# Performance work log

Measured on AMD Instinct MI355X. Metric: run time of the kernel, lower is better.

## Reference

```python
import jax, jax.numpy as jnp
import numpy as np

TOP_K = 2  # num_experts_per_tok


def setup_inputs() -> dict:
    key = jax.random.key(0)
    k1, k2, k3, k4 = jax.random.split(key, 4)
    T, H, I, E = 1024, 2048, 768, 8  # tokens, hidden, moe_intermediate, num_experts
    return {
        "hidden_states": jax.random.normal(k1, (T, H), jnp.float32),
        "gate_w": jax.random.normal(k2, (E, H), jnp.float32) * 0.02,      # router nn.Linear(H,E) weight
        "w_gate_up": jax.random.normal(k3, (E, 2 * I, H), jnp.float32) * 0.02,  # merged gate+up proj per expert
        "w_down": jax.random.normal(k4, (E, H, I), jnp.float32) * 0.02,   # down proj per expert
    }


def _moe(hidden_states, gate_w, w_gate_up, w_down):
    T, H = hidden_states.shape
    E = gate_w.shape[0]
    # router: softmax in fp32, then top-k, renormalize (matches _forward_local)
    logits = hidden_states @ gate_w.T                         # [T, E]
    probs = jax.nn.softmax(logits.astype(jnp.float32), axis=-1)
    top_w, top_i = jax.lax.top_k(probs, TOP_K)                # [T, K]
    top_w = top_w / jnp.sum(top_w, axis=-1, keepdims=True)
    top_w = top_w.astype(hidden_states.dtype)
    # per-token combine weight for each expert (top-k indices are unique per token)
    comb = jnp.zeros((T, E), hidden_states.dtype).at[
        jnp.arange(T)[:, None], top_i
    ].add(top_w)                                              # [T, E]

    def body(acc, xs):
        wgu, wd, cw = xs            # [2I,H], [H,I], [T]
        gu = hidden_states @ wgu.T  # [T, 2I]
        g, u = jnp.split(gu, 2, axis=-1)
        h = jax.nn.silu(g) * u      # SiluAndMul
        out = h @ wd.T              # [T, H]
        return acc + out * cw[:, None], None

    init = jnp.zeros_like(hidden_states)
    out, _ = jax.lax.scan(body, init, (w_gate_up, w_down, comb.T))
    return out


def reference(hidden_states, gate_w, w_gate_up, w_down):
    return _moe(hidden_states, gate_w, w_gate_up, w_down)
```

## Files before the change

kernel.cpp:

```cpp
#include <hip/hip_runtime.h>
#include <hip/hip_bf16.h>

typedef unsigned short u16;
typedef __bf16 bf16x8 __attribute__((ext_vector_type(8)));
typedef float f32x4 __attribute__((ext_vector_type(4)));

#define T_TOK 1024
#define HID   2048
#define IMM   768
#define NE    8
#define TWOI  1536
#define KTOT  6144

static __device__ __forceinline__ u16 f2bf(float f) {
  unsigned u = __float_as_uint(f);
  u += 0x7FFFu + ((u >> 16) & 1u);
  return (u16)(u >> 16);
}
static __device__ __forceinline__ float bf2f(u16 s) {
  return __uint_as_float(((unsigned)s) << 16);
}

__global__ __launch_bounds__(64) void router_kernel(
    const float* __restrict__ hid, const float* __restrict__ gw,
    float* __restrict__ comb)
{
  const int t = blockIdx.x;
  const int lane = threadIdx.x;
  float acc[NE];
#pragma unroll
  for (int e = 0; e < NE; ++e) acc[e] = 0.f;
  const float4* h4 = (const float4*)(hid + (long)t * HID);
#pragma unroll 2
  for (int c = lane; c < HID / 4; c += 64) {
    float4 x = h4[c];
#pragma unroll
    for (int e = 0; e < NE; ++e) {
      float4 w = ((const float4*)(gw + e * HID))[c];
      acc[e] += x.x * w.x + x.y * w.y + x.z * w.z + x.w * w.w;
    }
  }
#pragma unroll
  for (int e = 0; e < NE; ++e) {
    float v = acc[e];
#pragma unroll
    for (int off = 32; off > 0; off >>= 1) v += __shfl_xor(v, off, 64);
    acc[e] = v;
  }
  if (lane == 0) {
    float mx = acc[0];
#pragma unroll
    for (int e = 1; e < NE; ++e) mx = fmaxf(mx, acc[e]);
    float p[NE]; float s = 0.f;
#pragma unroll
    for (int e = 0; e < NE; ++e) { p[e] = expf(acc[e] - mx); s += p[e]; }
    const float inv = 1.f / s;
    float p1 = -1.f, p2 = -1.f; int i1 = 0, i2 = 0;
#pragma unroll
    for (int e = 0; e < NE; ++e) {
      float pe = p[e] * inv;
      if (pe > p1)      { p2 = p1; i2 = i1; p1 = pe; i1 = e; }
      else if (pe > p2) { p2 = pe; i2 = e; }
    }
    const float wsum = p1 + p2;
    float cw[NE];
#pragma unroll
    for (int e = 0; e < NE; ++e) cw[e] = 0.f;
    cw[i1] = p1 / wsum;
    cw[i2] = p2 / wsum;
#pragma unroll
    for (int e = 0; e < NE; ++e) comb[t * NE + e] = cw[e];
  }
}

__global__ __launch_bounds__(256) void cvt_kernel(
    const float* __restrict__ in, u16* __restrict__ out)
{
  const int i = blockIdx.x * 256 + threadIdx.x;
  float4 x = ((const float4*)in)[i];
  ushort4 o;
  o.x = f2bf(x.x); o.y = f2bf(x.y); o.z = f2bf(x.z); o.w = f2bf(x.w);
  ((ushort4*)out)[i] = o;
}

template<int K, bool OUT_ATOMIC>
__global__ __launch_bounds__(256, 2) void gemm_bt(
    const u16* __restrict__ A, int lda, long a_zoff,
    const float* __restrict__ B, long b_zoff,
    u16* __restrict__ Cb, float* __restrict__ Cf, int ldc, long c_zoff)
{
  constexpr int BM = 128, BN = 128, BK = 32;
  constexpr int LSTR = BK + 8;
  constexpr int NKT = K / BK;
  static_assert(NKT >= 2 && (K % BK) == 0, "K must be multiple of 32, >=64");
  __shared__ __align__(16) u16 As[2][BM * LSTR];
  __shared__ __align__(16) u16 Bs[2][BN * LSTR];

  const int tid  = threadIdx.x;
  const int lane = tid & 63;
  const int wave = tid >> 6;
  const int wm = wave >> 1, wn = wave & 1;
  const int lrow = lane & 15;
  const int lk   = (lane >> 4) << 3;

  const int z = blockIdx.z;
  const long m0 = (long)blockIdx.x * BM;
  const long n0 = (long)blockIdx.y * BN;

  const u16*   Ab = A + a_zoff * z + m0 * lda;
  const float* Bb = B + b_zoff * z + n0 * (long)K;

  const int r0  = tid >> 2;
  const int cs0 = (tid & 3) << 3;

  uint4 sa0, sa1; float4 sb0a, sb0b, sb1a, sb1b;

  auto gload = [&](int kk) {
    const u16* ap = Ab + (long)r0 * lda + kk + cs0;
    sa0 = *(const uint4*)ap;
    sa1 = *(const uint4*)(ap + 64l * lda);
    const float* bp = Bb + (long)r0 * K + kk + cs0;
    sb0a = *(const float4*)bp;
    sb0b = *(const float4*)(bp + 4);
    sb1a = *(const float4*)(bp + 64l * K);
    sb1b = *(const float4*)(bp + 64l * K + 4);
  };
  auto packb = [&](const float4& f0, const float4& f1) -> uint4 {
    return make_uint4(
      (unsigned)f2bf(f0.x) | ((unsigned)f2bf(f0.y) << 16),
      (unsigned)f2bf(f0.z) | ((unsigned)f2bf(f0.w) << 16),
      (unsigned)f2bf(f1.x) | ((unsigned)f2bf(f1.y) << 16),
      (unsigned)f2bf(f1.z) | ((unsigned)f2bf(f1.w) << 16));
  };
  auto swrite = [&](int buf) {
    *(uint4*)&As[buf][r0 * LSTR + cs0]        = sa0;
    *(uint4*)&As[buf][(r0 + 64) * LSTR + cs0] = sa1;
    *(uint4*)&Bs[buf][r0 * LSTR + cs0]        = packb(sb0a, sb0b);
    *(uint4*)&Bs[buf][(r0 + 64) * LSTR + cs0] = packb(sb1a, sb1b);
  };

  f32x4 acc[4][4];
  const f32x4 zero4 = {0.f, 0.f, 0.f, 0.f};
#pragma unroll
  for (int m = 0; m < 4; ++m)
#pragma unroll
    for (int n = 0; n < 4; ++n) acc[m][n] = zero4;

  auto compute = [&](int buf) {
    bf16x8 af[4], bfr[4];
#pragma unroll
    for (int m = 0; m < 4; ++m)
      af[m] = *(const bf16x8*)&As[buf][(wm * 64 + m * 16 + lrow) * LSTR + lk];
#pragma unroll
    for (int n = 0; n < 4; ++n)
      bfr[n] = *(const bf16x8*)&Bs[buf][(wn * 64 + n * 16 + lrow) * LSTR + lk];
#pragma unroll
    for (int m = 0; m < 4; ++m)
#pragma unroll
      for (int n = 0; n < 4; ++n)
        acc[m][n] = __builtin_amdgcn_mfma_f32_16x16x32_bf16(af[m], bfr[n], acc[m][n], 0, 0, 0);
  };

  gload(0);
  swrite(0);
  __syncthreads();
  int cur = 0;
#pragma unroll 1
  for (int kt = 0; kt < NKT - 1; ++kt) {
    gload((kt + 1) * BK);
    compute(cur);
    swrite(cur ^ 1);
    __syncthreads();
    cur ^= 1;
  }
  compute(cur);

  const long rbase = m0 + wm * 64 + ((lane >> 4) << 2);
  const long cbase = n0 + wn * 64 + lrow;
#pragma unroll
  for (int m = 0; m < 4; ++m) {
#pragma unroll
    for (int n = 0; n < 4; ++n) {
#pragma unroll
      for (int j = 0; j < 4; ++j) {
        const long row = rbase + m * 16 + j;
        const long col = cbase + n * 16;
        if constexpr (OUT_ATOMIC) {
          atomicAdd(Cf + c_zoff * z + row * ldc + col, acc[m][n][j]);
        } else {
          Cb[c_zoff * z + row * ldc + col] = f2bf(acc[m][n][j]);
        }
      }
    }
  }
}

__global__ __launch_bounds__(256) void silu_kernel(
    const u16* __restrict__ gu, const float* __restrict__ comb,
    u16* __restrict__ hp)
{
  const int c = blockIdx.x * 256 + threadIdx.x;
  const int o0 = c << 3;
  const int t = o0 / KTOT;
  const int r = o0 - t * KTOT;
  const int e = r / IMM;
  const int i0 = r - e * IMM;
  const u16* gp = gu + ((long)(e * T_TOK + t) * TWOI) + i0;
  uint4 gv = *(const uint4*)gp;
  uint4 uv = *(const uint4*)(gp + IMM);
  const float cw = comb[t * NE + e];
  const unsigned* gwv = (const unsigned*)&gv;
  const unsigned* uwv = (const unsigned*)&uv;
  unsigned outw[4];
#pragma unroll
  for (int q = 0; q < 4; ++q) {
    float g0 = bf2f((u16)(gwv[q] & 0xFFFFu));
    float g1 = bf2f((u16)(gwv[q] >> 16));
    float u0 = bf2f((u16)(uwv[q] & 0xFFFFu));
    float u1 = bf2f((u16)(uwv[q] >> 16));
    float h0 = cw * u0 * (g0 / (1.f + __expf(-g0)));
    float h1 = cw * u1 * (g1 / (1.f + __expf(-g1)));
    outw[q] = (unsigned)f2bf(h0) | ((unsigned)f2bf(h1) << 16);
  }
  *(uint4*)(hp + (long)o0) = make_uint4(outw[0], outw[1], outw[2], outw[3]);
}

extern "C" void kernel_launch(void* const* d_in, const int* in_sizes, int n_in,
                              void* d_out, int out_size, void* d_ws, size_t ws_size,
                              hipStream_t stream) {
  const float* hid = (const float*)d_in[0];
  const float* gw  = (const float*)d_in[1];
  const float* wgu = (const float*)d_in[2];
  const float* wd  = (const float*)d_in[3];
  float* out = (float*)d_out;

  char* ws = (char*)d_ws;
  u16*   hidb = (u16*)ws;
  float* comb = (float*)(ws + (4l << 20));
  u16*   gu   = (u16*)(ws + (4l << 20) + (1l << 15));
  u16*   hp   = (u16*)(ws + (4l << 20) + (1l << 15)
                          + (long)NE * T_TOK * TWOI * 2);

  hipMemsetAsync(d_out, 0, (size_t)out_size * sizeof(float), stream);
  router_kernel<<<T_TOK, 64, 0, stream>>>(hid, gw, comb);
  cvt_kernel<<<(T_TOK * HID / 4) / 256, 256, 0, stream>>>(hid, hidb);
  gemm_bt<HID, false><<<dim3(T_TOK / 128, TWOI / 128, NE), 256, 0, stream>>>(
      hidb, HID, 0, wgu, (long)TWOI * HID, gu, nullptr, TWOI, (long)T_TOK * TWOI);
  silu_kernel<<<(T_TOK * KTOT / 8) / 256, 256, 0, stream>>>(gu, comb, hp);
  gemm_bt<IMM, true><<<dim3(T_TOK / 128, HID / 128, NE), 256, 0, stream>>>(
      hp, KTOT, IMM, wd, (long)HID * IMM, nullptr, out, HID, 0);
}
```

Measured before the change: 382.1 us.

## Route tokens sparsely to experts with gathered grouped GEMMs instead of dense compute

The router now uses atomic counters to build per-expert token lists and per-slot combine weights, replacing the dense T×E combine matrix. The gate/up GEMM gathers only routed token rows, and grid tiles beyond each expert's count exit early. The SiLU stage works per slot, and the down GEMM scatters atomically into each token's output row. This removes the compute on tokens whose combine weight is zero, about three quarters of the GEMM work with top-2 of 8, at the cost of an extra memset, index indirection and possible load imbalance across experts.

```diff
diff --git a/kernel.cpp b/kernel.cpp
--- a/kernel.cpp
+++ b/kernel.cpp
@@ -10,7 +10,6 @@
 #define IMM   768
 #define NE    8
 #define TWOI  1536
-#define KTOT  6144
 
 static __device__ __forceinline__ u16 f2bf(float f) {
   unsigned u = __float_as_uint(f);
@@ -23,7 +22,7 @@
 
 __global__ __launch_bounds__(64) void router_kernel(
     const float* __restrict__ hid, const float* __restrict__ gw,
-    float* __restrict__ comb)
+    int* __restrict__ cnt, int* __restrict__ tok_of, float* __restrict__ wslot)
 {
   const int t = blockIdx.x;
   const int lane = threadIdx.x;
@@ -63,13 +62,12 @@
       else if (pe > p2) { p2 = pe; i2 = e; }
     }
     const float wsum = p1 + p2;
-    float cw[NE];
-#pragma unroll
-    for (int e = 0; e < NE; ++e) cw[e] = 0.f;
-    cw[i1] = p1 / wsum;
-    cw[i2] = p2 / wsum;
-#pragma unroll
-    for (int e = 0; e < NE; ++e) comb[t * NE + e] = cw[e];
+    int s1 = atomicAdd(&cnt[i1], 1);
+    tok_of[i1 * T_TOK + s1] = t;
+    wslot[i1 * T_TOK + s1] = p1 / wsum;
+    int s2 = atomicAdd(&cnt[i2], 1);
+    tok_of[i2 * T_TOK + s2] = t;
+    wslot[i2 * T_TOK + s2] = p2 / wsum;
   }
 }
 
@@ -83,16 +81,23 @@
   ((ushort4*)out)[i] = o;
 }
 
-template<int K, bool OUT_ATOMIC>
-__global__ __launch_bounds__(256, 2) void gemm_bt(
+template<int K, bool GATHER_A, bool OUT_ATOMIC>
+__global__ __launch_bounds__(256, 2) void gemm_moe(
     const u16* __restrict__ A, int lda, long a_zoff,
     const float* __restrict__ B, long b_zoff,
+    const int* __restrict__ tok_of, const int* __restrict__ cnt,
     u16* __restrict__ Cb, float* __restrict__ Cf, int ldc, long c_zoff)
 {
   constexpr int BM = 128, BN = 128, BK = 32;
   constexpr int LSTR = BK + 8;
   constexpr int NKT = K / BK;
   static_assert(NKT >= 2 && (K % BK) == 0, "K must be multiple of 32, >=64");
+
+  const int z = blockIdx.z;
+  const int nrow = cnt[z];
+  const long m0 = (long)blockIdx.x * BM;
+  if (m0 >= nrow) return;
+
   __shared__ __align__(16) u16 As[2][BM * LSTR];
   __shared__ __align__(16) u16 Bs[2][BN * LSTR];
 
@@ -103,22 +108,26 @@
   const int lrow = lane & 15;
   const int lk   = (lane >> 4) << 3;
 
-  const int z = blockIdx.z;
-  const long m0 = (long)blockIdx.x * BM;
   const long n0 = (long)blockIdx.y * BN;
-
-  const u16*   Ab = A + a_zoff * z + m0 * lda;
   const float* Bb = B + b_zoff * z + n0 * (long)K;
 
   const int r0  = tid >> 2;
   const int cs0 = (tid & 3) << 3;
 
+  const u16 *ap0, *ap1;
+  if constexpr (GATHER_A) {
+    ap0 = A + (long)tok_of[z * T_TOK + m0 + r0] * lda + cs0;
+    ap1 = A + (long)tok_of[z * T_TOK + m0 + r0 + 64] * lda + cs0;
+  } else {
+    ap0 = A + a_zoff * z + (m0 + r0) * (long)lda + cs0;
+    ap1 = ap0 + 64l * lda;
+  }
+
   uint4 sa0, sa1; float4 sb0a, sb0b, sb1a, sb1b;
 
   auto gload = [&](int kk) {
-    const u16* ap = Ab + (long)r0 * lda + kk + cs0;
-    sa0 = *(const uint4*)ap;
-    sa1 = *(const uint4*)(ap + 64l * lda);
+    sa0 = *(const uint4*)(ap0 + kk);
+    sa1 = *(const uint4*)(ap1 + kk);
     const float* bp = Bb + (long)r0 * K + kk + cs0;
     sb0a = *(const float4*)bp;
     sb0b = *(const float4*)(bp + 4);
@@ -175,7 +184,7 @@
   }
   compute(cur);
 
-  const long rbase = m0 + wm * 64 + ((lane >> 4) << 2);
+  const int rloc = wm * 64 + ((lane >> 4) << 2);
   const long cbase = n0 + wn * 64 + lrow;
 #pragma unroll
   for (int m = 0; m < 4; ++m) {
@@ -183,12 +192,15 @@
     for (int n = 0; n < 4; ++n) {
 #pragma unroll
       for (int j = 0; j < 4; ++j) {
-        const long row = rbase + m * 16 + j;
+        const long slot = m0 + rloc + m * 16 + j;
         const long col = cbase + n * 16;
         if constexpr (OUT_ATOMIC) {
-          atomicAdd(Cf + c_zoff * z + row * ldc + col, acc[m][n][j]);
+          if (slot < nrow) {
+            const long tok = tok_of[z * T_TOK + slot];
+            atomicAdd(Cf + tok * ldc + col, acc[m][n][j]);
+          }
         } else {
-          Cb[c_zoff * z + row * ldc + col] = f2bf(acc[m][n][j]);
+          Cb[c_zoff * z + slot * ldc + col] = f2bf(acc[m][n][j]);
         }
       }
     }
@@ -196,19 +208,17 @@
 }
 
 __global__ __launch_bounds__(256) void silu_kernel(
-    const u16* __restrict__ gu, const float* __restrict__ comb,
+    const u16* __restrict__ gu, const float* __restrict__ wslot,
     u16* __restrict__ hp)
 {
   const int c = blockIdx.x * 256 + threadIdx.x;
-  const int o0 = c << 3;
-  const int t = o0 / KTOT;
-  const int r = o0 - t * KTOT;
-  const int e = r / IMM;
-  const int i0 = r - e * IMM;
-  const u16* gp = gu + ((long)(e * T_TOK + t) * TWOI) + i0;
+  const int idx = c << 3;
+  const int g = idx / IMM;
+  const int i0 = idx - g * IMM;
+  const u16* gp = gu + (long)g * TWOI + i0;
   uint4 gv = *(const uint4*)gp;
   uint4 uv = *(const uint4*)(gp + IMM);
-  const float cw = comb[t * NE + e];
+  const float cw = wslot[g];
   const unsigned* gwv = (const unsigned*)&gv;
   const unsigned* uwv = (const unsigned*)&uv;
   unsigned outw[4];
@@ -222,7 +232,7 @@
     float h1 = cw * u1 * (g1 / (1.f + __expf(-g1)));
     outw[q] = (unsigned)f2bf(h0) | ((unsigned)f2bf(h1) << 16);
   }
-  *(uint4*)(hp + (long)o0) = make_uint4(outw[0], outw[1], outw[2], outw[3]);
+  *(uint4*)(hp + (long)g * IMM + i0) = make_uint4(outw[0], outw[1], outw[2], outw[3]);
 }
 
 extern "C" void kernel_launch(void* const* d_in, const int* in_sizes, int n_in,
@@ -235,18 +245,24 @@
   float* out = (float*)d_out;
 
   char* ws = (char*)d_ws;
-  u16*   hidb = (u16*)ws;
-  float* comb = (float*)(ws + (4l << 20));
-  u16*   gu   = (u16*)(ws + (4l << 20) + (1l << 15));
-  u16*   hp   = (u16*)(ws + (4l << 20) + (1l << 15)
-                          + (long)NE * T_TOK * TWOI * 2);
+  u16*   hidb   = (u16*)ws;
+  int*   cnt    = (int*)(ws + (4l << 20));
+  int*   tok_of = (int*)(ws + (4l << 20) + (1l << 12));
+  float* wslot  = (float*)(ws + (4l << 20) + (1l << 12) + (1l << 15));
+  u16*   gu     = (u16*)(ws + (4l << 20) + (1l << 17));
+  u16*   hp     = (u16*)(ws + (4l << 20) + (1l << 17)
+                            + (long)NE * T_TOK * TWOI * 2);
 
   hipMemsetAsync(d_out, 0, (size_t)out_size * sizeof(float), stream);
-  router_kernel<<<T_TOK, 64, 0, stream>>>(hid, gw, comb);
+  hipMemsetAsync(ws + (4l << 20), 0, (1l << 17), stream);
+
+  router_kernel<<<T_TOK, 64, 0, stream>>>(hid, gw, cnt, tok_of, wslot);
   cvt_kernel<<<(T_TOK * HID / 4) / 256, 256, 0, stream>>>(hid, hidb);
-  gemm_bt<HID, false><<<dim3(T_TOK / 128, TWOI / 128, NE), 256, 0, stream>>>(
-      hidb, HID, 0, wgu, (long)TWOI * HID, gu, nullptr, TWOI, (long)T_TOK * TWOI);
-  silu_kernel<<<(T_TOK * KTOT / 8) / 256, 256, 0, stream>>>(gu, comb, hp);
-  gemm_bt<IMM, true><<<dim3(T_TOK / 128, HID / 128, NE), 256, 0, stream>>>(
-      hp, KTOT, IMM, wd, (long)HID * IMM, nullptr, out, HID, 0);
-}
+  gemm_moe<HID, true, false><<<dim3(T_TOK / 128, TWOI / 128, NE), 256, 0, stream>>>(
+      hidb, HID, 0, wgu, (long)TWOI * HID,
+      tok_of, cnt, gu, nullptr, TWOI, (long)T_TOK * TWOI);
+  silu_kernel<<<(NE * T_TOK * IMM / 8) / 256, 256, 0, stream>>>(gu, wslot, hp);
+  gemm_moe<IMM, false, true><<<dim3(T_TOK / 128, HID / 128, NE), 256, 0, stream>>>(
+      hp, IMM, (long)T_TOK * IMM, wd, (long)HID * IMM,
+      tok_of, cnt, nullptr, out, HID, 0);
+}
```

Result: no change. 386.6 us (+1.2%).
